# Optimization experiments

Hardware: AMD Instinct MI355X
Metric: run time of the kernel (lower is better)

Reference implementation:

```python
import jax, jax.numpy as jnp
import numpy as np

B, Himg, Wimg, DIM = 8, 128, 128, 256
HEADS = 16            # d_head = DIM // HEADS = 16 == HEADS (required by temperature broadcast)
HW = Himg * Wimg


def setup_inputs() -> dict:
    key = jax.random.key(0)
    ks = jax.random.split(key, 9)
    s = 0.02
    return {
        "x": jax.random.normal(ks[0], (B, Himg, Wimg, DIM), jnp.float32),
        "w_qkv": jax.random.normal(ks[1], (DIM, 3 * DIM), jnp.float32) * s,
        "w_dw": jax.random.normal(ks[2], (3, 3, 1, 3 * DIM), jnp.float32) * s,  # HWIO, depthwise
        "w_out": jax.random.normal(ks[3], (DIM, DIM), jnp.float32) * s,
        "temperature": jnp.ones((1, 1, HEADS), jnp.float32),
        "mean_q": jax.random.normal(ks[4], (1, 1, HW, 1), jnp.float32) * 0.05,
        "var_q": 0.5 + jax.random.uniform(ks[5], (1, 1, HW, 1), jnp.float32),
        "mean_k": jax.random.normal(ks[6], (1, 1, HW, 1), jnp.float32) * 0.05,
        "var_k": 0.5 + jax.random.uniform(ks[7], (1, 1, HW, 1), jnp.float32),
    }


def _to_heads(t, b, hw, heads):
    # (b,h,w,heads*dh) -> (b, heads, h*w, dh)
    return t.reshape(b, hw, heads, -1).transpose(0, 2, 1, 3)


def reference(x, w_qkv, w_dw, w_out, temperature, mean_q, var_q, mean_k, var_k):
    b, h, w, c = x.shape
    heads = temperature.shape[-1]
    # pointwise QKV projection (1x1 conv, no bias)
    qkv = jnp.einsum('bhwc,cd->bhwd', x, w_qkv)
    # depthwise 3x3 conv, groups = 3*dim, 'same' padding
    qkv = jax.lax.conv_general_dilated(
        qkv, w_dw, window_strides=(1, 1), padding='SAME',
        dimension_numbers=('NHWC', 'HWIO', 'NHWC'),
        feature_group_count=3 * c)
    q, k, v = jnp.split(qkv, 3, axis=-1)
    q = _to_heads(q, b, h * w, heads)  # (b, heads, hw, dh)
    k = _to_heads(k, b, h * w, heads)
    v = _to_heads(v, b, h * w, heads)
    # keras Normalization(axis=-2): per-spatial-position mean/variance
    q = (q - mean_q) * jax.lax.rsqrt(var_q)
    k = (k - mean_k) * jax.lax.rsqrt(var_k)
    # channel attention: k^T @ q over spatial axis -> (b, heads, dh, dh)
    attn = jnp.einsum('bnsi,bnsj->bnij', k, q)
    attn = attn * temperature  # broadcasts over last axis (dh == heads)
    attn = jax.nn.softmax(attn, axis=-2)
    out = jnp.einsum('bnsd,bndj->bnsj', v, attn)  # v @ attn
    # (b, heads, hw, dh) -> (b, h, w, heads*dh)
    out = out.transpose(0, 2, 1, 3).reshape(b, h, w, c)
    out = jnp.einsum('bhwc,cd->bhwd', out, w_out)
    return out
```

## Files before the change

kernel.cpp:

```cpp
#include <hip/hip_runtime.h>
#include <cstdint>
#include <cstddef>

#define NB    8
#define HWSZ  16384
#define DIM   256
#define NCH   128
#define CHSZ  (HWSZ / NCH)

typedef short bf16x8 __attribute__((ext_vector_type(8)));
typedef float f32x4 __attribute__((ext_vector_type(4)));
typedef unsigned short u16;
typedef u16 u16x8 __attribute__((ext_vector_type(8)));

__device__ __forceinline__ float bf2f(u16 u) {
    union { uint32_t i; float f; } w; w.i = ((uint32_t)u) << 16; return w.f;
}
__device__ __forceinline__ u16 f2bf(float f) {
    union { float f; uint32_t i; } w; w.f = f;
    uint32_t x = w.i;
    return (u16)((x + 0x7fffu + ((x >> 16) & 1u)) >> 16);
}

__device__ __forceinline__ void gload_lds16(const u16* g, u16* l) {
    __builtin_amdgcn_global_load_lds(
        (const __attribute__((address_space(1))) uint32_t*)g,
        (__attribute__((address_space(3))) uint32_t*)l, 16, 0, 0);
}

__global__ void transpose_w32(const float* __restrict__ in, u16* __restrict__ out,
                              int K, int N) {
    int t = blockIdx.x * 256 + threadIdx.x;
    if (t < K * N) {
        int kk = t / N;
        int n  = t % N;
        out[(size_t)n * K + kk] = f2bf(in[t]);
    }
}

__global__ void conv_bf16(const float* __restrict__ in, u16* __restrict__ out,
                          int n8) {
    int t = blockIdx.x * 256 + threadIdx.x;
    if (t < n8) {
        const float4* p = (const float4*)(in + (size_t)t * 8);
        float4 a = p[0], b = p[1];
        u16x8 o;
        o[0] = f2bf(a.x); o[1] = f2bf(a.y); o[2] = f2bf(a.z); o[3] = f2bf(a.w);
        o[4] = f2bf(b.x); o[5] = f2bf(b.y); o[6] = f2bf(b.z); o[7] = f2bf(b.w);
        *(u16x8*)(out + (size_t)t * 8) = o;
    }
}

#define GEMM_BODY(STORE_STMT)                                                   \
    __shared__ u16 At[128 * 32];                                                \
    __shared__ u16 Bl[128 * 32];                                                \
    const int nwg = gridDim.x * gridDim.y;                                      \
    const int bid = blockIdx.y * gridDim.x + blockIdx.x;                        \
    const int swz = (bid & 7) * (nwg >> 3) + (bid >> 3);                        \
    const int bx  = swz % gridDim.x;                                            \
    const int by  = swz / gridDim.x;                                            \
    const int t    = threadIdx.x;                                               \
    const int lane = t & 63;                                                    \
    const int wave = t >> 6;                                                    \
    const int r16  = lane & 15;                                                 \
    const int quad = lane >> 4;                                                 \
    const int m0   = by * 128;                                                  \
    const int n0   = bx * 128;                                                  \
    const int K    = 256;                                                       \
    const int wm   = (wave >> 1) * 64;                                          \
    const int wn   = (wave & 1) * 64;                                           \
    f32x4 acc[4][4];                                                            \
    _Pragma("unroll")                                                           \
    for (int mi = 0; mi < 4; ++mi)                                              \
        _Pragma("unroll")                                                       \
        for (int ni = 0; ni < 4; ++ni)                                          \
            acc[mi][ni] = (f32x4){0.f, 0.f, 0.f, 0.f};                          \
    const int srow = t >> 2;                \
    const int skc  = (t & 3) * 8;                         \
    for (int kk = 0; kk < K; kk += 32) {                                        \
        if (kk) __syncthreads();                                                \
        _Pragma("unroll")                                                       \
        for (int it = 0; it < 2; ++it) {                                        \
            int c   = t + it * 256;                                             \
            int row = srow + it * 64;                                           \
            gload_lds16(A  + (size_t)(m0 + row) * K + kk + skc, At + c * 8);    \
            gload_lds16(Bt + (size_t)(n0 + row) * K + kk + skc, Bl + c * 8);    \
        }                                                                       \
        __syncthreads();                                                        \
        bf16x8 af[4], bfr[4];                                                   \
        _Pragma("unroll")                                                       \
        for (int mi = 0; mi < 4; ++mi)                                          \
            af[mi] = *(const bf16x8*)(At + (wm + mi * 16 + r16) * 32 + quad * 8);\
        _Pragma("unroll")                                                       \
        for (int ni = 0; ni < 4; ++ni)                                          \
            bfr[ni] = *(const bf16x8*)(Bl + (wn + ni * 16 + r16) * 32 + quad * 8);\
        _Pragma("unroll")                                                       \
        for (int mi = 0; mi < 4; ++mi)                                          \
            _Pragma("unroll")                                                   \
            for (int ni = 0; ni < 4; ++ni)                                      \
                acc[mi][ni] = __builtin_amdgcn_mfma_f32_16x16x32_bf16(          \
                    af[mi], bfr[ni], acc[mi][ni], 0, 0, 0);                     \
    }                                                                           \
    _Pragma("unroll")                                                           \
    for (int mi = 0; mi < 4; ++mi)                                              \
        _Pragma("unroll")                                                       \
        for (int ni = 0; ni < 4; ++ni)                                          \
            _Pragma("unroll")                                                   \
            for (int r = 0; r < 4; ++r) {                                       \
                int m = m0 + wm + mi * 16 + quad * 4 + r;                       \
                int n = n0 + wn + ni * 16 + r16;                                \
                STORE_STMT;                                                     \
            }

__global__ __launch_bounds__(256) void gemm_lds_cbf(const u16* __restrict__ A,
                                                    const u16* __restrict__ Bt,
                                                    u16* __restrict__ C, int N) {
    GEMM_BODY(C[(size_t)m * N + n] = f2bf(acc[mi][ni][r]))
}

__global__ __launch_bounds__(256) void gemm_lds_cf32(const u16* __restrict__ A,
                                                     const u16* __restrict__ Bt,
                                                     float* __restrict__ C, int N) {
    GEMM_BODY(C[(size_t)m * N + n] = acc[mi][ni][r])
}

#define DW_LOADROW(buf, I)                                                      \
    {                                                                           \
        const int  rowy_ = y0 - 1 + (I);                                        \
        const int  rowc_ = rowy_ < 0 ? 0 : (rowy_ > 127 ? 127 : rowy_);         \
        const u16* rp_ = qkv + ((size_t)b * HWSZ + rowc_ * 128 + x) * 768 + c0; \
        buf[0] = *(const u16x8*)(rp_ - 768);                                    \
        buf[1] = *(const u16x8*)(rp_);                                          \
        buf[2] = *(const u16x8*)(rp_ + 768);                                    \
    }

#define DW_CONSUME(buf, I)                                                      \
    {                                                                           \
        const int  rowy_ = y0 - 1 + (I);                                        \
        const bool rok_  = (unsigned)rowy_ < 128u;                              \
        u16x8 a0 = (rok_ && xlok) ? buf[0] : vz;                                \
        u16x8 a1 = rok_           ? buf[1] : vz;                                \
        u16x8 a2 = (rok_ && xrok) ? buf[2] : vz;                                \
        float f0[8], f1[8], f2[8];                                              \
        _Pragma("unroll")                                                       \
        for (int c = 0; c < 8; ++c) {                                           \
            f0[c] = bf2f(a0[c]); f1[c] = bf2f(a1[c]); f2[c] = bf2f(a2[c]);      \
        }                                                                       \
        _Pragma("unroll")                                                       \
        for (int r = 0; r < 4; ++r) {                                           \
            if (r < (I) - 2 || r > (I)) continue;      \
            const int tr = ((I) - r) * 3;                         \
            _Pragma("unroll")                                                   \
            for (int c = 0; c < 8; ++c) {                                       \
                acc[r][c] += f0[c] * w[tr + 0][c];                              \
                acc[r][c] += f1[c] * w[tr + 1][c];                              \
                acc[r][c] += f2[c] * w[tr + 2][c];                              \
            }                                                                   \
        }                                                                       \
    }

__global__ __launch_bounds__(192) void dwconv_norm(
        const u16* __restrict__ qkv, const float* __restrict__ wdw,
        const float* __restrict__ mq, const float* __restrict__ vq,
        const float* __restrict__ mk, const float* __restrict__ vk,
        u16* __restrict__ qo, u16* __restrict__ ko, u16* __restrict__ vo) {
    const int t    = threadIdx.x;
    const int g    = t % 96;
    const int c0   = g * 8;
    const int xcol = t / 96;
    const int x    = blockIdx.x * 2 + xcol;
    const int y0   = blockIdx.y * 4;
    const int b    = blockIdx.z;

    float w[9][8];
#pragma unroll
    for (int kt = 0; kt < 9; ++kt) {
        float4 w0 = *(const float4*)(wdw + (size_t)kt * 768 + c0);
        float4 w1 = *(const float4*)(wdw + (size_t)kt * 768 + c0 + 4);
        w[kt][0] = w0.x; w[kt][1] = w0.y; w[kt][2] = w0.z; w[kt][3] = w0.w;
        w[kt][4] = w1.x; w[kt][5] = w1.y; w[kt][6] = w1.z; w[kt][7] = w1.w;
    }

    float acc[4][8];
#pragma unroll
    for (int r = 0; r < 4; ++r)
#pragma unroll
        for (int c = 0; c < 8; ++c) acc[r][c] = 0.f;

    const bool xlok = (x > 0);
    const bool xrok = (x < 127);
    const u16x8 vz = {0, 0, 0, 0, 0, 0, 0, 0};

    u16x8 bufA[3], bufB[3], bufC[3];
    DW_LOADROW(bufA, 0)
    DW_LOADROW(bufB, 1)
    DW_LOADROW(bufC, 2)
    DW_CONSUME(bufA, 0)
    DW_LOADROW(bufA, 3)
    DW_CONSUME(bufB, 1)
    DW_LOADROW(bufB, 4)
    DW_CONSUME(bufC, 2)
    DW_LOADROW(bufC, 5)
    DW_CONSUME(bufA, 3)
    DW_CONSUME(bufB, 4)
    DW_CONSUME(bufC, 5)

    const int seg = c0 >> 8;
    const int cc  = c0 & 255;
#pragma unroll
    for (int r = 0; r < 4; ++r) {
        const int    s  = (y0 + r) * 128 + x;
        const size_t p  = (size_t)b * HWSZ + s;
        const size_t op = p * 256 + cc;
        u16x8 o;
        if (seg == 0) {
            float m = mq[s], rs = rsqrtf(vq[s]);
#pragma unroll
            for (int c = 0; c < 8; ++c) o[c] = f2bf((acc[r][c] - m) * rs);
            *(u16x8*)(qo + op) = o;
        } else if (seg == 1) {
            float m = mk[s], rs = rsqrtf(vk[s]);
#pragma unroll
            for (int c = 0; c < 8; ++c) o[c] = f2bf((acc[r][c] - m) * rs);
            *(u16x8*)(ko + op) = o;
        } else {
#pragma unroll
            for (int c = 0; c < 8; ++c) o[c] = f2bf(acc[r][c]);
            *(u16x8*)(vo + op) = o;
        }
    }
}

__global__ __launch_bounds__(256) void attn_mfma(
        const u16* __restrict__ q, const u16* __restrict__ k,
        float* __restrict__ attn_ps, int nbn) {
    __shared__ u16 qt[32 * 256];
    __shared__ u16 kt[32 * 256];
    const int b    = blockIdx.x;
    const int ch   = blockIdx.y;
    const int t    = threadIdx.x;
    const int wave = t >> 6;
    const int lane = t & 63;
    const int r16  = lane & 15;
    const int quad = lane >> 4;
    const size_t base = (size_t)b * HWSZ * 256;
    const int sBeg = ch * CHSZ;

    f32x4 acc[4];
#pragma unroll
    for (int i = 0; i < 4; ++i) acc[i] = (f32x4){0.f, 0.f, 0.f, 0.f};

    for (int s0 = sBeg; s0 < sBeg + CHSZ; s0 += 32) {
        __syncthreads();
#pragma unroll
        for (int r = 0; r < 4; ++r) {
            int c   = t + r * 256;
            int row = c >> 5;
            int c32 = c & 31;
            int pcol = (c32 * 8) ^ ((row >> 3) << 4);
            *(u16x8*)(&qt[row * 256 + pcol]) =
                *(const u16x8*)(q + base + (size_t)(s0 + row) * 256 + c32 * 8);
            *(u16x8*)(&kt[row * 256 + pcol]) =
                *(const u16x8*)(k + base + (size_t)(s0 + row) * 256 + c32 * 8);
        }
        __syncthreads();
#pragma unroll
        for (int h4 = 0; h4 < 4; ++h4) {
            int h   = wave * 4 + h4;
            int pc  = (h * 16 + r16) ^ (quad << 4);
            u16x8 ak, aq;
#pragma unroll
            for (int e = 0; e < 8; ++e) {
                int addr = (quad * 8 + e) * 256 + pc;
                ak[e] = kt[addr];
                aq[e] = qt[addr];
            }
            acc[h4] = __builtin_amdgcn_mfma_f32_16x16x32_bf16(
                (bf16x8)ak, (bf16x8)aq, acc[h4], 0, 0, 0);
        }
    }

#pragma unroll
    for (int h4 = 0; h4 < 4; ++h4) {
        int h  = wave * 4 + h4;
        int bn = b * 16 + h;
#pragma unroll
        for (int r = 0; r < 4; ++r) {
            attn_ps[((size_t)ch * nbn + bn) * 256 + (quad * 4 + r) * 16 + r16] =
                acc[h4][r];
        }
    }
}

__global__ void reduce_attn(const float* __restrict__ ps,
                            float* __restrict__ out, int n) {
    int t = blockIdx.x * 256 + threadIdx.x;
    if (t < n) {
        float s = 0.f;
        for (int c = 0; c < NCH; ++c) s += ps[(size_t)c * n + t];
        out[t] = s;
    }
}

__global__ __launch_bounds__(64) void softmax_attn(
        const float* __restrict__ attn, const float* __restrict__ temp,
        float* __restrict__ attn_sm) {
    int bn = blockIdx.x;
    int j  = threadIdx.x;
    if (j >= 16) return;
    float tj = temp[j];
    float vals[16];
    float mx = -3.4e38f;
#pragma unroll
    for (int i = 0; i < 16; ++i) {
        vals[i] = attn[bn * 256 + i * 16 + j] * tj;
        mx = fmaxf(mx, vals[i]);
    }
    float sum = 0.f;
#pragma unroll
    for (int i = 0; i < 16; ++i) {
        vals[i] = expf(vals[i] - mx);
        sum += vals[i];
    }
    float inv = 1.f / sum;
#pragma unroll
    for (int i = 0; i < 16; ++i)
        attn_sm[bn * 256 + i * 16 + j] = vals[i] * inv;
}

__global__ __launch_bounds__(256) void apply_attn(
        const u16* __restrict__ v, const float* __restrict__ attn_sm,
        u16* __restrict__ out_mid) {
    __shared__ float alds[16 * 257];
    const int tid = threadIdx.x;
    const int t   = blockIdx.x * 256 + tid;
    const int n   = t & 15;
    const int p   = t >> 4;
    const int b   = p >> 14;

#pragma unroll
    for (int r = 0; r < 16; ++r) {
        int idx = r * 256 + tid;
        alds[(idx >> 8) * 257 + (idx & 255)] = attn_sm[(size_t)b * 4096 + idx];
    }
    __syncthreads();

    const u16* vp = v + (size_t)p * 256 + n * 16;
    u16x8 v0 = *(const u16x8*)vp;
    u16x8 v1 = *(const u16x8*)(vp + 8);
    float vv[16];
#pragma unroll
    for (int i = 0; i < 8; ++i) { vv[i] = bf2f(v0[i]); vv[8 + i] = bf2f(v1[i]); }

    const float* am = &alds[n * 257];
    float o[16];
#pragma unroll
    for (int j = 0; j < 16; ++j) o[j] = 0.f;
#pragma unroll
    for (int d = 0; d < 16; ++d) {
        float vd = vv[d];
#pragma unroll
        for (int j = 0; j < 16; ++j) o[j] += vd * am[d * 16 + j];
    }

    u16x8 o0, o1;
#pragma unroll
    for (int i = 0; i < 8; ++i) { o0[i] = f2bf(o[i]); o1[i] = f2bf(o[8 + i]); }
    u16* outp = out_mid + (size_t)p * 256 + n * 16;
    *(u16x8*)outp       = o0;
    *(u16x8*)(outp + 8) = o1;
}

extern "C" void kernel_launch(void* const* d_in, const int* in_sizes, int n_in,
                              void* d_out, int out_size, void* d_ws, size_t ws_size,
                              hipStream_t stream) {
    const float* x     = (const float*)d_in[0];
    const float* wqkv  = (const float*)d_in[1];
    const float* wdw   = (const float*)d_in[2];
    const float* wout  = (const float*)d_in[3];
    const float* temp  = (const float*)d_in[4];
    const float* mq    = (const float*)d_in[5];
    const float* vq    = (const float*)d_in[6];
    const float* mk    = (const float*)d_in[7];
    const float* vk    = (const float*)d_in[8];
    float* out_f = (float*)d_out;

    char* ws = (char*)d_ws;
    u16*   btq      = (u16*)ws;
    u16*   bto      = (u16*)(ws + 768 * 256 * 2);
    char*  dynb     = ws + 768 * 256 * 2 + 256 * 256 * 2;
    const size_t FIXED = (size_t)(768 * 256 * 2 + 256 * 256 * 2);

    const size_t PER_IMG = (size_t)HWSZ * 768 * 2 + 3 * (size_t)HWSZ * 256 * 2
                         + 2 * 4096 * 4;
    int CB = 8;
    while (CB > 1 && FIXED + (size_t)CB * PER_IMG > ws_size) CB >>= 1;

    transpose_w32<<<(256 * 768 + 255) / 256, 256, 0, stream>>>(wqkv, btq, 256, 768);
    transpose_w32<<<(256 * 256 + 255) / 256, 256, 0, stream>>>(wout, bto, 256, 256);

    const size_t QKVB = (size_t)CB * HWSZ * 768 * 2;
    const size_t SEGB = (size_t)CB * HWSZ * 256 * 2;
    u16*   qkv_c    = (u16*)dynb;
    u16*   qb       = (u16*)(dynb + QKVB);
    u16*   kb       = (u16*)(dynb + QKVB + SEGB);
    u16*   vb       = (u16*)(dynb + QKVB + 2 * SEGB);
    float* attn_raw = (float*)(dynb + QKVB + 3 * SEGB);
    float* attn_sm  = attn_raw + (size_t)CB * 4096;
    u16*   om_c     = qkv_c;
    u16*   xb       = qb;
    float* attn_ps  = (float*)qkv_c;

    const int rowsC = CB * HWSZ;
    const int nbn   = CB * 16;
    for (int b0 = 0; b0 < NB; b0 += CB) {
        const float* xc   = x + (size_t)b0 * HWSZ * 256;
        float*       outc = out_f + (size_t)b0 * HWSZ * 256;

        conv_bf16<<<(rowsC * 32 + 255) / 256, 256, 0, stream>>>(xc, xb, rowsC * 32);

        gemm_lds_cbf<<<dim3(768 / 128, rowsC / 128), 256, 0, stream>>>(xb, btq,
                                                                       qkv_c, 768);
        dwconv_norm<<<dim3(64, 32, CB), 192, 0, stream>>>(qkv_c, wdw,
                                                          mq, vq, mk, vk,
                                                          qb, kb, vb);
        attn_mfma<<<dim3(CB, NCH), 256, 0, stream>>>(qb, kb, attn_ps, nbn);
        reduce_attn<<<(CB * 4096 + 255) / 256, 256, 0, stream>>>(attn_ps, attn_raw,
                                                                 CB * 4096);
        softmax_attn<<<CB * 16, 64, 0, stream>>>(attn_raw, temp, attn_sm);

        apply_attn<<<(rowsC * 16) / 256, 256, 0, stream>>>(vb, attn_sm, om_c);

        gemm_lds_cf32<<<dim3(256 / 128, rowsC / 128), 256, 0, stream>>>(om_c, bto,
                                                                        outc, 256);
    }
}
```

Measured before the change: 607.1 us.

## Fuse input bf16 conversion into QKV GEMM and merge attention reduce with softmax

The QKV GEMM now loads fp32 x straight into LDS and converts to bf16 at fragment-read time, which removes the separate conv_bf16 pass and its bf16 round trip through global memory. The attention partial-sum reduction and the softmax are merged into one kernel launched per (batch, head), dropping one launch and the intermediate raw-attention buffer. The depthwise conv issues all six row loads before any consumption, separated by a scheduling barrier, to raise memory-level parallelism. The trade-offs are twice the A-tile LDS traffic with conversion work repeated across the N tiles, more registers in the dwconv kernel, and a lightly parallel reduce (64 threads per block).

```diff
diff --git a/kernel.cpp b/kernel.cpp
--- a/kernel.cpp
+++ b/kernel.cpp
@@ -1,4 +1,5 @@
 #include <hip/hip_runtime.h>
+#include <hip/hip_bf16.h>
 #include <cstdint>
 #include <cstddef>
 
@@ -21,8 +22,18 @@
     uint32_t x = w.i;
     return (u16)((x + 0x7fffu + ((x >> 16) & 1u)) >> 16);
 }
+__device__ __forceinline__ u16 f2bf_hw(float f) {
+    union { __hip_bfloat16 h; u16 u; } cv;
+    cv.h = __float2bfloat16(f);
+    return cv.u;
+}
 
 __device__ __forceinline__ void gload_lds16(const u16* g, u16* l) {
+    __builtin_amdgcn_global_load_lds(
+        (const __attribute__((address_space(1))) uint32_t*)g,
+        (__attribute__((address_space(3))) uint32_t*)l, 16, 0, 0);
+}
+__device__ __forceinline__ void gload_lds16f(const float* g, float* l) {
     __builtin_amdgcn_global_load_lds(
         (const __attribute__((address_space(1))) uint32_t*)g,
         (__attribute__((address_space(3))) uint32_t*)l, 16, 0, 0);
@@ -38,90 +49,150 @@
     }
 }
 
-__global__ void conv_bf16(const float* __restrict__ in, u16* __restrict__ out,
-                          int n8) {
-    int t = blockIdx.x * 256 + threadIdx.x;
-    if (t < n8) {
-        const float4* p = (const float4*)(in + (size_t)t * 8);
-        float4 a = p[0], b = p[1];
-        u16x8 o;
-        o[0] = f2bf(a.x); o[1] = f2bf(a.y); o[2] = f2bf(a.z); o[3] = f2bf(a.w);
-        o[4] = f2bf(b.x); o[5] = f2bf(b.y); o[6] = f2bf(b.z); o[7] = f2bf(b.w);
-        *(u16x8*)(out + (size_t)t * 8) = o;
-    }
-}
-
-#define GEMM_BODY(STORE_STMT)                                                   \
-    __shared__ u16 At[128 * 32];                                                \
-    __shared__ u16 Bl[128 * 32];                                                \
-    const int nwg = gridDim.x * gridDim.y;                                      \
-    const int bid = blockIdx.y * gridDim.x + blockIdx.x;                        \
-    const int swz = (bid & 7) * (nwg >> 3) + (bid >> 3);                        \
-    const int bx  = swz % gridDim.x;                                            \
-    const int by  = swz / gridDim.x;                                            \
-    const int t    = threadIdx.x;                                               \
-    const int lane = t & 63;                                                    \
-    const int wave = t >> 6;                                                    \
-    const int r16  = lane & 15;                                                 \
-    const int quad = lane >> 4;                                                 \
-    const int m0   = by * 128;                                                  \
-    const int n0   = bx * 128;                                                  \
-    const int K    = 256;                                                       \
-    const int wm   = (wave >> 1) * 64;                                          \
-    const int wn   = (wave & 1) * 64;                                           \
-    f32x4 acc[4][4];                                                            \
-    _Pragma("unroll")                                                           \
-    for (int mi = 0; mi < 4; ++mi)                                              \
-        _Pragma("unroll")                                                       \
-        for (int ni = 0; ni < 4; ++ni)                                          \
-            acc[mi][ni] = (f32x4){0.f, 0.f, 0.f, 0.f};                          \
-    const int srow = t >> 2;                \
-    const int skc  = (t & 3) * 8;                         \
-    for (int kk = 0; kk < K; kk += 32) {                                        \
-        if (kk) __syncthreads();                                                \
-        _Pragma("unroll")                                                       \
-        for (int it = 0; it < 2; ++it) {                                        \
-            int c   = t + it * 256;                                             \
-            int row = srow + it * 64;                                           \
-            gload_lds16(A  + (size_t)(m0 + row) * K + kk + skc, At + c * 8);    \
-            gload_lds16(Bt + (size_t)(n0 + row) * K + kk + skc, Bl + c * 8);    \
-        }                                                                       \
-        __syncthreads();                                                        \
-        bf16x8 af[4], bfr[4];                                                   \
-        _Pragma("unroll")                                                       \
-        for (int mi = 0; mi < 4; ++mi)                                          \
-            af[mi] = *(const bf16x8*)(At + (wm + mi * 16 + r16) * 32 + quad * 8);\
-        _Pragma("unroll")                                                       \
-        for (int ni = 0; ni < 4; ++ni)                                          \
-            bfr[ni] = *(const bf16x8*)(Bl + (wn + ni * 16 + r16) * 32 + quad * 8);\
-        _Pragma("unroll")                                                       \
-        for (int mi = 0; mi < 4; ++mi)                                          \
-            _Pragma("unroll")                                                   \
-            for (int ni = 0; ni < 4; ++ni)                                      \
-                acc[mi][ni] = __builtin_amdgcn_mfma_f32_16x16x32_bf16(          \
-                    af[mi], bfr[ni], acc[mi][ni], 0, 0, 0);                     \
-    }                                                                           \
-    _Pragma("unroll")                                                           \
-    for (int mi = 0; mi < 4; ++mi)                                              \
-        _Pragma("unroll")                                                       \
-        for (int ni = 0; ni < 4; ++ni)                                          \
-            _Pragma("unroll")                                                   \
-            for (int r = 0; r < 4; ++r) {                                       \
-                int m = m0 + wm + mi * 16 + quad * 4 + r;                       \
-                int n = n0 + wn + ni * 16 + r16;                                \
-                STORE_STMT;                                                     \
+__global__ __launch_bounds__(256) void gemm_xf32_cbf(const float* __restrict__ A,
+                                                     const u16* __restrict__ Bt,
+                                                     u16* __restrict__ C, int N) {
+    __shared__ float Af[128 * 32];
+    __shared__ u16   Bl[128 * 32];
+    const int nwg = gridDim.x * gridDim.y;
+    const int bid = blockIdx.y * gridDim.x + blockIdx.x;
+    const int swz = (bid & 7) * (nwg >> 3) + (bid >> 3);
+    const int bx  = swz % gridDim.x;
+    const int by  = swz / gridDim.x;
+    const int t    = threadIdx.x;
+    const int lane = t & 63;
+    const int wave = t >> 6;
+    const int r16  = lane & 15;
+    const int quad = lane >> 4;
+    const int m0   = by * 128;
+    const int n0   = bx * 128;
+    const int K    = 256;
+    const int wm   = (wave >> 1) * 64;
+    const int wn   = (wave & 1) * 64;
+
+    f32x4 acc[4][4];
+#pragma unroll
+    for (int mi = 0; mi < 4; ++mi)
+#pragma unroll
+        for (int ni = 0; ni < 4; ++ni)
+            acc[mi][ni] = (f32x4){0.f, 0.f, 0.f, 0.f};
+
+    const int srowB = t >> 2;
+    const int skcB  = (t & 3) * 8;
+    const int srowA = t >> 3;
+    const int skcA  = (t & 7) * 4;
+
+    for (int kk = 0; kk < K; kk += 32) {
+        if (kk) __syncthreads();
+#pragma unroll
+        for (int it = 0; it < 4; ++it) {
+            int row = srowA + it * 32;
+            gload_lds16f(A + (size_t)(m0 + row) * K + kk + skcA,
+                         Af + row * 32 + skcA);
+        }
+#pragma unroll
+        for (int it = 0; it < 2; ++it) {
+            int row = srowB + it * 64;
+            gload_lds16(Bt + (size_t)(n0 + row) * K + kk + skcB,
+                        Bl + (t + it * 256) * 8);
+        }
+        __syncthreads();
+        bf16x8 af[4], bfr[4];
+#pragma unroll
+        for (int mi = 0; mi < 4; ++mi) {
+            const float* ap = Af + (wm + mi * 16 + r16) * 32 + quad * 8;
+            f32x4 a0 = *(const f32x4*)ap;
+            f32x4 a1 = *(const f32x4*)(ap + 4);
+            u16x8 au;
+#pragma unroll
+            for (int e = 0; e < 4; ++e) { au[e] = f2bf_hw(a0[e]); au[4 + e] = f2bf_hw(a1[e]); }
+            af[mi] = (bf16x8)au;
+        }
+#pragma unroll
+        for (int ni = 0; ni < 4; ++ni)
+            bfr[ni] = *(const bf16x8*)(Bl + (wn + ni * 16 + r16) * 32 + quad * 8);
+#pragma unroll
+        for (int mi = 0; mi < 4; ++mi)
+#pragma unroll
+            for (int ni = 0; ni < 4; ++ni)
+                acc[mi][ni] = __builtin_amdgcn_mfma_f32_16x16x32_bf16(
+                    af[mi], bfr[ni], acc[mi][ni], 0, 0, 0);
+    }
+
+#pragma unroll
+    for (int mi = 0; mi < 4; ++mi)
+#pragma unroll
+        for (int ni = 0; ni < 4; ++ni)
+#pragma unroll
+            for (int r = 0; r < 4; ++r) {
+                int m = m0 + wm + mi * 16 + quad * 4 + r;
+                int n = n0 + wn + ni * 16 + r16;
+                C[(size_t)m * N + n] = f2bf(acc[mi][ni][r]);
             }
-
-__global__ __launch_bounds__(256) void gemm_lds_cbf(const u16* __restrict__ A,
-                                                    const u16* __restrict__ Bt,
-                                                    u16* __restrict__ C, int N) {
-    GEMM_BODY(C[(size_t)m * N + n] = f2bf(acc[mi][ni][r]))
 }
 
 __global__ __launch_bounds__(256) void gemm_lds_cf32(const u16* __restrict__ A,
                                                      const u16* __restrict__ Bt,
                                                      float* __restrict__ C, int N) {
-    GEMM_BODY(C[(size_t)m * N + n] = acc[mi][ni][r])
+    __shared__ u16 At[128 * 32];
+    __shared__ u16 Bl[128 * 32];
+    const int nwg = gridDim.x * gridDim.y;
+    const int bid = blockIdx.y * gridDim.x + blockIdx.x;
+    const int swz = (bid & 7) * (nwg >> 3) + (bid >> 3);
+    const int bx  = swz % gridDim.x;
+    const int by  = swz / gridDim.x;
+    const int t    = threadIdx.x;
+    const int lane = t & 63;
+    const int wave = t >> 6;
+    const int r16  = lane & 15;
+    const int quad = lane >> 4;
+    const int m0   = by * 128;
+    const int n0   = bx * 128;
+    const int K    = 256;
+    const int wm   = (wave >> 1) * 64;
+    const int wn   = (wave & 1) * 64;
+    f32x4 acc[4][4];
+#pragma unroll
+    for (int mi = 0; mi < 4; ++mi)
+#pragma unroll
+        for (int ni = 0; ni < 4; ++ni)
+            acc[mi][ni] = (f32x4){0.f, 0.f, 0.f, 0.f};
+    const int srow = t >> 2;
+    const int skc  = (t & 3) * 8;
+    for (int kk = 0; kk < K; kk += 32) {
+        if (kk) __syncthreads();
+#pragma unroll
+        for (int it = 0; it < 2; ++it) {
+            int c   = t + it * 256;
+            int row = srow + it * 64;
+            gload_lds16(A  + (size_t)(m0 + row) * K + kk + skc, At + c * 8);
+            gload_lds16(Bt + (size_t)(n0 + row) * K + kk + skc, Bl + c * 8);
+        }
+        __syncthreads();
+        bf16x8 af[4], bfr[4];
+#pragma unroll
+        for (int mi = 0; mi < 4; ++mi)
+            af[mi] = *(const bf16x8*)(At + (wm + mi * 16 + r16) * 32 + quad * 8);
+#pragma unroll
+        for (int ni = 0; ni < 4; ++ni)
+            bfr[ni] = *(const bf16x8*)(Bl + (wn + ni * 16 + r16) * 32 + quad * 8);
+#pragma unroll
+        for (int mi = 0; mi < 4; ++mi)
+#pragma unroll
+            for (int ni = 0; ni < 4; ++ni)
+                acc[mi][ni] = __builtin_amdgcn_mfma_f32_16x16x32_bf16(
+                    af[mi], bfr[ni], acc[mi][ni], 0, 0, 0);
+    }
+#pragma unroll
+    for (int mi = 0; mi < 4; ++mi)
+#pragma unroll
+        for (int ni = 0; ni < 4; ++ni)
+#pragma unroll
+            for (int r = 0; r < 4; ++r) {
+                int m = m0 + wm + mi * 16 + quad * 4 + r;
+                int n = n0 + wn + ni * 16 + r16;
+                C[(size_t)m * N + n] = acc[mi][ni][r];
+            }
 }
 
 #define DW_LOADROW(buf, I)                                                      \
@@ -191,19 +262,20 @@
     const bool xrok = (x < 127);
     const u16x8 vz = {0, 0, 0, 0, 0, 0, 0, 0};
 
-    u16x8 bufA[3], bufB[3], bufC[3];
-    DW_LOADROW(bufA, 0)
-    DW_LOADROW(bufB, 1)
-    DW_LOADROW(bufC, 2)
-    DW_CONSUME(bufA, 0)
-    DW_LOADROW(bufA, 3)
-    DW_CONSUME(bufB, 1)
-    DW_LOADROW(bufB, 4)
-    DW_CONSUME(bufC, 2)
-    DW_LOADROW(bufC, 5)
-    DW_CONSUME(bufA, 3)
-    DW_CONSUME(bufB, 4)
-    DW_CONSUME(bufC, 5)
+    u16x8 tap[6][3];
+    DW_LOADROW(tap[0], 0)
+    DW_LOADROW(tap[1], 1)
+    DW_LOADROW(tap[2], 2)
+    DW_LOADROW(tap[3], 3)
+    DW_LOADROW(tap[4], 4)
+    DW_LOADROW(tap[5], 5)
+    __builtin_amdgcn_sched_barrier(0);
+    DW_CONSUME(tap[0], 0)
+    DW_CONSUME(tap[1], 1)
+    DW_CONSUME(tap[2], 2)
+    DW_CONSUME(tap[3], 3)
+    DW_CONSUME(tap[4], 4)
+    DW_CONSUME(tap[5], 5)
 
     const int seg = c0 >> 8;
     const int cc  = c0 & 255;
@@ -292,40 +364,42 @@
     }
 }
 
-__global__ void reduce_attn(const float* __restrict__ ps,
-                            float* __restrict__ out, int n) {
-    int t = blockIdx.x * 256 + threadIdx.x;
-    if (t < n) {
-        float s = 0.f;
-        for (int c = 0; c < NCH; ++c) s += ps[(size_t)c * n + t];
-        out[t] = s;
-    }
-}
-
-__global__ __launch_bounds__(64) void softmax_attn(
-        const float* __restrict__ attn, const float* __restrict__ temp,
-        float* __restrict__ attn_sm) {
-    int bn = blockIdx.x;
-    int j  = threadIdx.x;
-    if (j >= 16) return;
-    float tj = temp[j];
-    float vals[16];
-    float mx = -3.4e38f;
-#pragma unroll
-    for (int i = 0; i < 16; ++i) {
-        vals[i] = attn[bn * 256 + i * 16 + j] * tj;
-        mx = fmaxf(mx, vals[i]);
-    }
-    float sum = 0.f;
-#pragma unroll
-    for (int i = 0; i < 16; ++i) {
-        vals[i] = expf(vals[i] - mx);
-        sum += vals[i];
-    }
-    float inv = 1.f / sum;
-#pragma unroll
-    for (int i = 0; i < 16; ++i)
-        attn_sm[bn * 256 + i * 16 + j] = vals[i] * inv;
+__global__ __launch_bounds__(64) void reduce_softmax(
+        const float* __restrict__ ps, const float* __restrict__ temp,
+        float* __restrict__ attn_sm, int nbn) {
+    __shared__ float sl[256];
+    const int bn = blockIdx.x;
+    const int t  = threadIdx.x;
+
+    f32x4 s = (f32x4){0.f, 0.f, 0.f, 0.f};
+    for (int ch = 0; ch < NCH; ++ch) {
+        const f32x4 v = *(const f32x4*)(ps + ((size_t)ch * nbn + bn) * 256 + t * 4);
+        s += v;
+    }
+    *(f32x4*)(sl + t * 4) = s;
+    __syncthreads();
+
+    if (t < 16) {
+        const int j = t;
+        float tj = temp[j];
+        float vals[16];
+        float mx = -3.4e38f;
+#pragma unroll
+        for (int i = 0; i < 16; ++i) {
+            vals[i] = sl[i * 16 + j] * tj;
+            mx = fmaxf(mx, vals[i]);
+        }
+        float sum = 0.f;
+#pragma unroll
+        for (int i = 0; i < 16; ++i) {
+            vals[i] = expf(vals[i] - mx);
+            sum += vals[i];
+        }
+        float inv = 1.f / sum;
+#pragma unroll
+        for (int i = 0; i < 16; ++i)
+            attn_sm[bn * 256 + i * 16 + j] = vals[i] * inv;
+    }
 }
 
 __global__ __launch_bounds__(256) void apply_attn(
@@ -405,10 +479,8 @@
     u16*   qb       = (u16*)(dynb + QKVB);
     u16*   kb       = (u16*)(dynb + QKVB + SEGB);
     u16*   vb       = (u16*)(dynb + QKVB + 2 * SEGB);
-    float* attn_raw = (float*)(dynb + QKVB + 3 * SEGB);
-    float* attn_sm  = attn_raw + (size_t)CB * 4096;
+    float* attn_sm  = (float*)(dynb + QKVB + 3 * SEGB);
     u16*   om_c     = qkv_c;
-    u16*   xb       = qb;
     float* attn_ps  = (float*)qkv_c;
 
     const int rowsC = CB * HWSZ;
@@ -417,17 +489,13 @@
         const float* xc   = x + (size_t)b0 * HWSZ * 256;
         float*       outc = out_f + (size_t)b0 * HWSZ * 256;
 
-        conv_bf16<<<(rowsC * 32 + 255) / 256, 256, 0, stream>>>(xc, xb, rowsC * 32);
-
-        gemm_lds_cbf<<<dim3(768 / 128, rowsC / 128), 256, 0, stream>>>(xb, btq,
-                                                                       qkv_c, 768);
+        gemm_xf32_cbf<<<dim3(768 / 128, rowsC / 128), 256, 0, stream>>>(xc, btq,
+                                                                        qkv_c, 768);
         dwconv_norm<<<dim3(64, 32, CB), 192, 0, stream>>>(qkv_c, wdw,
                                                           mq, vq, mk, vk,
                                                           qb, kb, vb);
         attn_mfma<<<dim3(CB, NCH), 256, 0, stream>>>(qb, kb, attn_ps, nbn);
-        reduce_attn<<<(CB * 4096 + 255) / 256, 256, 0, stream>>>(attn_ps, attn_raw,
-                                                                 CB * 4096);
-        softmax_attn<<<CB * 16, 64, 0, stream>>>(attn_raw, temp, attn_sm);
+        reduce_softmax<<<nbn, 64, 0, stream>>>(attn_ps, temp, attn_sm, nbn);
 
         apply_attn<<<(rowsC * 16) / 256, 256, 0, stream>>>(vb, attn_sm, om_c);
 
```

Measured after the change: 614.6 us. No clear change (+1.2%).
